# Performance work log

Measured on AMD Instinct MI355X. Metric: run time of the kernel, lower is better.

Reference implementation:

```python
import jax, jax.numpy as jnp
import numpy as np

N_NODES = 50000
N_EDGES = 500000
ATOM_DIM = 128
BOND_DIM = 64
EMB = 128
N_GRAPHS = 256
NUM_LAYER = 2


def _kaiming_uniform(key, fan_out, fan_in):
    # kaiming_uniform_ with nonlinearity='relu': bound = sqrt(6 / fan_in) * sqrt(2)/1 adjustments
    gain = np.sqrt(2.0)
    bound = gain * np.sqrt(3.0 / fan_in)
    return jax.random.uniform(key, (fan_out, fan_in), jnp.float32, -bound, bound)


def setup_inputs() -> dict:
    key = jax.random.key(0)
    ks = jax.random.split(key, 12)
    x = jax.random.normal(ks[0], (N_NODES, ATOM_DIM), jnp.float32)
    edge_attr = jax.random.normal(ks[1], (N_EDGES, BOND_DIM), jnp.float32)
    edge_index = jax.random.randint(ks[2], (2, N_EDGES), 0, N_NODES, jnp.int64)
    batch = jnp.sort(jax.random.randint(ks[3], (N_NODES,), 0, N_GRAPHS, jnp.int64))
    Wa = _kaiming_uniform(ks[4], EMB, ATOM_DIM)
    ba = jnp.zeros((EMB,), jnp.float32)
    Wb = _kaiming_uniform(ks[5], EMB, BOND_DIM)
    bb = jnp.zeros((EMB,), jnp.float32)
    W1 = _kaiming_uniform(ks[6], EMB, EMB)
    b1 = jnp.zeros((EMB,), jnp.float32)
    W2 = _kaiming_uniform(ks[7], EMB // 2, EMB)
    b2 = jnp.zeros((EMB // 2,), jnp.float32)
    W3 = _kaiming_uniform(ks[8], 1, EMB // 2)
    return {"x": x, "edge_attr": edge_attr, "edge_index": edge_index, "batch": batch,
            "Wa": Wa, "ba": ba, "Wb": Wb, "bb": bb,
            "W1": W1, "b1": b1, "W2": W2, "b2": b2, "W3": W3}


def reference(x, edge_attr, edge_index, batch, Wa, ba, Wb, bb, W1, b1, W2, b2, W3):
    src, dst = edge_index[0], edge_index[1]
    # Step 1: embeddings
    node_emb = x @ Wa.T + ba          # [N, EMB]
    edge_emb = edge_attr @ Wb.T + bb  # [E, EMB]
    # Step 2: message passing layers: gather, multiply with edge_emb, scatter-add, residual
    for _ in range(NUM_LAYER):
        msg = node_emb[src] * edge_emb                           # [E, EMB]
        agg = jax.ops.segment_sum(msg, dst, num_segments=N_NODES)  # [N, EMB]
        node_emb = node_emb + agg
    # Step 3: energy MLP (ReLU first, per nn.Sequential)
    h = jax.nn.relu(node_emb)
    h = jax.nn.relu(h @ W1.T + b1)
    h = jax.nn.relu(h @ W2.T + b2)
    node_energy = h @ W3.T            # [N, 1], no bias
    # Step 4: global add pool over graphs
    dg = jax.ops.segment_sum(node_energy, batch, num_segments=N_GRAPHS)  # [G, 1]
    return dg
```

## Files before the change

kernel.cpp:

```cpp
#include <hip/hip_runtime.h>
#include <cstdio>
#include <cstdint>

#define N_NODES 50000
#define N_EDGES 500000
#define EMB 128
#define BOND 64
#define NGRAPH 256
#define NB_SCAN ((N_NODES + 255) / 256)
#define NSTRIP (N_NODES / 16)
#define ESTRIP (N_EDGES / 16)
#define NCHUNK (N_EDGES * BOND / 8)

typedef short bf16x8 __attribute__((ext_vector_type(8)));
typedef unsigned short u16x8 __attribute__((ext_vector_type(8)));
typedef float f32x4  __attribute__((ext_vector_type(4)));

__device__ __forceinline__ unsigned short f2bf(float v){
  unsigned u = __float_as_uint(v);
  unsigned r = (u + 0x7fffu + ((u >> 16) & 1u)) >> 16;
  return (unsigned short)r;
}
__device__ __forceinline__ float bf2f(unsigned short u){
  return __uint_as_float(((unsigned)u) << 16);
}
__device__ __forceinline__ unsigned short brelu(unsigned short u){
  return (u & 0x8000u) ? (unsigned short)0 : u;
}


__global__ void prep_w(const float* __restrict__ Wa, const float* __restrict__ W1,
                       const float* __restrict__ W2, const float* __restrict__ Wb,
                       unsigned short* __restrict__ wabf, unsigned short* __restrict__ w1bf,
                       unsigned short* __restrict__ w2bf, unsigned short* __restrict__ wbbf)
{
  int i = blockIdx.x * 256 + threadIdx.x;
  if (i < 40960){
    int i2 = i & 16383;
    int j = i2 & 7, lb = (i2 >> 3) & 63, kc = (i2 >> 9) & 3, tn = i2 >> 11;
    int lm = lb & 15, q = lb >> 4;
    int row = tn * 16 + lm, col = kc * 32 + q * 8 + j;
    if (i < 16384){
      wabf[i] = f2bf(Wa[row * EMB + col]);
    } else if (i < 32768){
      int pcol = j * 16 + kc * 4 + q;
      w1bf[i2] = f2bf(W1[row * EMB + pcol]);
    } else {
      w2bf[i2] = f2bf(W2[row * EMB + col]);
    }
  } else if (i < 49152){
    int i2 = i - 40960;
    int j = i2 & 7, l = (i2 >> 3) & 63, kc = (i2 >> 9) & 1, tn = i2 >> 10;
    int lm = l & 15, q = l >> 4;
    wbbf[i2] = f2bf(Wb[(tn * 16 + lm) * BOND + kc * 32 + q * 8 + j]);
  }
}

__global__ __launch_bounds__(256) void node_gemm_mfma(const float* __restrict__ x,
    const unsigned short* __restrict__ wabf, const float* __restrict__ ba,
    unsigned short* __restrict__ out)
{
  const int t = threadIdx.x;
  const int wv = t >> 6, l = t & 63;
  const int lm = l & 15, q = l >> 4;
  union U8 { bf16x8 v; unsigned short s[8]; };
  const int strip = blockIdx.x * 4 + wv;
  if (strip >= NSTRIP) return;
  const long n0 = (long)strip * 16;

  bf16x8 a[4];
  #pragma unroll
  for (int kc = 0; kc < 4; kc++){
    const float* ap = x + (n0 + lm) * (long)EMB + kc * 32 + q * 8;
    float4 x0 = *(const float4*)ap;
    float4 x1 = *(const float4*)(ap + 4);
    U8 u;
    u.s[0] = f2bf(x0.x); u.s[1] = f2bf(x0.y); u.s[2] = f2bf(x0.z); u.s[3] = f2bf(x0.w);
    u.s[4] = f2bf(x1.x); u.s[5] = f2bf(x1.y); u.s[6] = f2bf(x1.z); u.s[7] = f2bf(x1.w);
    a[kc] = u.v;
  }
  float biasv[8];
  #pragma unroll
  for (int tn = 0; tn < 8; tn++) biasv[tn] = ba[tn * 16 + lm];

  f32x4 acc[8];
  #pragma unroll
  for (int tn = 0; tn < 8; tn++) acc[tn] = (f32x4){0.f, 0.f, 0.f, 0.f};
  #pragma unroll
  for (int kc = 0; kc < 4; kc++){
    #pragma unroll
    for (int tn = 0; tn < 8; tn++){
      bf16x8 bf = *(const bf16x8*)(wabf + (size_t)((tn * 4 + kc) * 64 + l) * 8);
      acc[tn] = __builtin_amdgcn_mfma_f32_16x16x32_bf16(a[kc], bf, acc[tn], 0, 0, 0);
    }
  }
  #pragma unroll
  for (int i = 0; i < 4; i++){
    U8 o;
    #pragma unroll
    for (int tn = 0; tn < 8; tn++) o.s[tn] = f2bf(acc[tn][i] + biasv[tn]);
    *(bf16x8*)(out + (n0 + q * 4 + i) * (long)EMB + lm * 8) = o.v;
  }
}

__global__ __launch_bounds__(256) void edge_gemm_mfma(
    const unsigned short* __restrict__ attr_bf, const unsigned short* __restrict__ wbbf,
    const float* __restrict__ bb, const int2* __restrict__ cse,
    unsigned short* __restrict__ eemb)
{
  const int t = threadIdx.x;
  const int l = t & 63;
  const int lm = l & 15, q = l >> 4;
  union U8 { bf16x8 v; unsigned short s[8]; };

  bf16x8 bfrag[8][2];
  float bias[8];
  #pragma unroll
  for (int tn = 0; tn < 8; tn++){
    bias[tn] = bb[tn * 16 + lm];
    #pragma unroll
    for (int kc = 0; kc < 2; kc++)
      bfrag[tn][kc] = *(const bf16x8*)(wbbf + (size_t)((tn * 2 + kc) * 64 + l) * 8);
  }

  const long wid = (long)blockIdx.x * 4 + (t >> 6);
  const long stride = (long)gridDim.x * 4 * 16;
  for (long p0 = wid * 16; p0 < N_EDGES; p0 += stride){
    long eid = (long)cse[p0 + lm].y;
    bf16x8 af0 = *(const bf16x8*)(attr_bf + eid * BOND + q * 8);
    bf16x8 af1 = *(const bf16x8*)(attr_bf + eid * BOND + 32 + q * 8);
    f32x4 acc[8];
    #pragma unroll
    for (int tn = 0; tn < 8; tn++) acc[tn] = (f32x4){0.f, 0.f, 0.f, 0.f};
    #pragma unroll
    for (int tn = 0; tn < 8; tn++){
      acc[tn] = __builtin_amdgcn_mfma_f32_16x16x32_bf16(af0, bfrag[tn][0], acc[tn], 0, 0, 0);
      acc[tn] = __builtin_amdgcn_mfma_f32_16x16x32_bf16(af1, bfrag[tn][1], acc[tn], 0, 0, 0);
    }
    #pragma unroll
    for (int i = 0; i < 4; i++){
      U8 o;
      #pragma unroll
      for (int tn = 0; tn < 8; tn++) o.s[tn] = f2bf(acc[tn][i] + bias[tn]);
      *(bf16x8*)(eemb + (p0 + q * 4 + i) * (long)EMB + lm * 8) = o.v;
    }
  }
}


__global__ __launch_bounds__(256) void count_deg_conv(const int* __restrict__ ei,
    int* __restrict__ deg, const float* __restrict__ attr,
    unsigned short* __restrict__ attr_bf)
{
  int id = blockIdx.x * 256 + threadIdx.x;
  if (id < N_EDGES) atomicAdd(&deg[ei[N_EDGES + id]], 1);
  const float* s = attr + (size_t)id * 8;
  float4 a0 = *(const float4*)s;
  float4 a1 = *(const float4*)(s + 4);
  u16x8 o;
  o[0] = f2bf(a0.x); o[1] = f2bf(a0.y); o[2] = f2bf(a0.z); o[3] = f2bf(a0.w);
  o[4] = f2bf(a1.x); o[5] = f2bf(a1.y); o[6] = f2bf(a1.z); o[7] = f2bf(a1.w);
  *(u16x8*)(attr_bf + (size_t)id * 8) = o;
}

__global__ __launch_bounds__(256) void scan_s1(const int* __restrict__ deg,
                                               int* __restrict__ blocksum)
{
  int i = blockIdx.x * 256 + threadIdx.x;
  int lane = threadIdx.x & 63, w = threadIdx.x >> 6;
  int v = (i < N_NODES) ? deg[i] : 0;
  #pragma unroll
  for (int o = 32; o > 0; o >>= 1) v += __shfl_down(v, o, 64);
  __shared__ int ws4[4];
  if (lane == 0) ws4[w] = v;
  __syncthreads();
  if (threadIdx.x == 0) blocksum[blockIdx.x] = ws4[0] + ws4[1] + ws4[2] + ws4[3];
}

__global__ __launch_bounds__(256) void scan_s2(const int* __restrict__ blocksum,
                                               int* __restrict__ blockoff,
                                               int* __restrict__ off)
{
  int t = threadIdx.x;
  int lane = t & 63, w = t >> 6;
  int v = (t < NB_SCAN) ? blocksum[t] : 0;
  int x = v;
  #pragma unroll
  for (int d = 1; d < 64; d <<= 1){
    int y = __shfl_up(x, d, 64);
    if (lane >= d) x += y;
  }
  __shared__ int wsum[4];
  if (lane == 63) wsum[w] = x;
  __syncthreads();
  int wo = 0;
  for (int j = 0; j < w; j++) wo += wsum[j];
  if (t < NB_SCAN) blockoff[t] = wo + x - v;
  if (t == 0) off[N_NODES] = wsum[0] + wsum[1] + wsum[2] + wsum[3];
}

__global__ __launch_bounds__(256) void scan_s3(const int* __restrict__ deg,
    const int* __restrict__ blockoff, int* __restrict__ off, int* __restrict__ fill)
{
  int i = blockIdx.x * 256 + threadIdx.x;
  int lane = threadIdx.x & 63, w = threadIdx.x >> 6;
  int v = (i < N_NODES) ? deg[i] : 0;
  int x = v;
  #pragma unroll
  for (int d = 1; d < 64; d <<= 1){
    int y = __shfl_up(x, d, 64);
    if (lane >= d) x += y;
  }
  __shared__ int wsum[4];
  if (lane == 63) wsum[w] = x;
  __syncthreads();
  int wo = 0;
  for (int j = 0; j < w; j++) wo += wsum[j];
  if (i < N_NODES){
    int excl = blockoff[blockIdx.x] + wo + x - v;
    off[i] = excl;
    fill[i] = excl;
  }
}

__global__ __launch_bounds__(256) void scatter_edges(const int* __restrict__ ei,
    int* __restrict__ fill, int2* __restrict__ cse)
{
  int e = blockIdx.x * 256 + threadIdx.x;
  if (e < N_EDGES){
    int dst = ei[N_EDGES + e];
    int p = atomicAdd(&fill[dst], 1);
    cse[p] = make_int2(ei[e], e);
  }
}

__global__ __launch_bounds__(256) void agg_kernel(const unsigned short* __restrict__ node_old,
    const unsigned short* __restrict__ eemb, const int* __restrict__ off,
    const int2* __restrict__ cse, unsigned short* __restrict__ node_new)
{
  int n = blockIdx.x * 8 + (threadIdx.x >> 5);
  if (n >= N_NODES) return;
  int c0 = (threadIdx.x & 31) * 4;
  int s = off[n], e = off[n + 1];
  ushort4 r = *(const ushort4*)(node_old + (long)n * EMB + c0);
  float4 accA = make_float4(bf2f(r.x), bf2f(r.y), bf2f(r.z), bf2f(r.w));
  float4 accB = make_float4(0.f, 0.f, 0.f, 0.f);
  int i = s;

#define AGG_BLOCK(CNT)                                                        \
  {                                                                           \
    int idx[CNT];                                                             \
    _Pragma("unroll")                                                         \
    for (int j = 0; j < CNT; j++) idx[j] = cse[i + j].x;                      \
    ushort4 a[CNT], eb[CNT];                                                  \
    _Pragma("unroll")                                                         \
    for (int j = 0; j < CNT; j++){                                            \
      a[j]  = *(const ushort4*)(node_old + (long)idx[j] * EMB + c0);          \
      eb[j] = *(const ushort4*)(eemb + (long)(i + j) * EMB + c0);             \
    }                                                                         \
    _Pragma("unroll")                                                         \
    for (int j = 0; j < CNT; j++){                                            \
      float4& acc = (j & 1) ? accB : accA;                                    \
      acc.x = fmaf(bf2f(a[j].x), bf2f(eb[j].x), acc.x);                       \
      acc.y = fmaf(bf2f(a[j].y), bf2f(eb[j].y), acc.y);                       \
      acc.z = fmaf(bf2f(a[j].z), bf2f(eb[j].z), acc.z);                       \
      acc.w = fmaf(bf2f(a[j].w), bf2f(eb[j].w), acc.w);                       \
    }                                                                         \
    i += CNT;                                                                 \
  }

  for (; i + 8 <= e; ) AGG_BLOCK(8)
  if (i + 4 <= e) AGG_BLOCK(4)
  if (i + 2 <= e) AGG_BLOCK(2)
  if (i < e) AGG_BLOCK(1)
#undef AGG_BLOCK

  ushort4 o;
  o.x = f2bf(accA.x + accB.x);
  o.y = f2bf(accA.y + accB.y);
  o.z = f2bf(accA.z + accB.z);
  o.w = f2bf(accA.w + accB.w);
  *(ushort4*)(node_new + (long)n * EMB + c0) = o;
}

__global__ __launch_bounds__(256) void mlp_mfma_pool(const unsigned short* __restrict__ ne,
    const unsigned short* __restrict__ w1bf, const unsigned short* __restrict__ w2bf,
    const float* __restrict__ b1, const float* __restrict__ b2,
    const float* __restrict__ W3, const int* __restrict__ batch,
    float* __restrict__ dg)
{
  __shared__ float h1s[4][16 * 132];
  __shared__ float pool[NGRAPH];
  const int t = threadIdx.x;
  const int wv = t >> 6, l = t & 63;
  const int lm = l & 15, q = l >> 4;
  union U8 { bf16x8 v; unsigned short s[8]; };

  for (int i = t; i < NGRAPH; i += 256) pool[i] = 0.f;
  __syncthreads();

  const int strip = blockIdx.x * 4 + wv;
  if (strip < NSTRIP){
    const long n0 = (long)strip * 16;

    float b1v[8], b2v[4], w3v[4];
    #pragma unroll
    for (int tn = 0; tn < 8; tn++) b1v[tn] = b1[tn * 16 + lm];
    #pragma unroll
    for (int tc = 0; tc < 4; tc++){ b2v[tc] = b2[tc * 16 + lm]; w3v[tc] = W3[tc * 16 + lm]; }

    bf16x8 a1[4];
    #pragma unroll
    for (int kc = 0; kc < 4; kc++){
      const unsigned short* ap = ne + (n0 + lm) * (long)EMB + kc * 32 + q * 8;
      ushort4 v0 = *(const ushort4*)ap;
      ushort4 v1 = *(const ushort4*)(ap + 4);
      U8 u;
      u.s[0] = brelu(v0.x); u.s[1] = brelu(v0.y); u.s[2] = brelu(v0.z); u.s[3] = brelu(v0.w);
      u.s[4] = brelu(v1.x); u.s[5] = brelu(v1.y); u.s[6] = brelu(v1.z); u.s[7] = brelu(v1.w);
      a1[kc] = u.v;
    }

    f32x4 acc1[8];
    #pragma unroll
    for (int tn = 0; tn < 8; tn++) acc1[tn] = (f32x4){b1v[tn], b1v[tn], b1v[tn], b1v[tn]};
    #pragma unroll
    for (int kc = 0; kc < 4; kc++){
      #pragma unroll
      for (int tn = 0; tn < 8; tn++){
        bf16x8 bf = *(const bf16x8*)(w1bf + (size_t)((tn * 4 + kc) * 64 + l) * 8);
        acc1[tn] = __builtin_amdgcn_mfma_f32_16x16x32_bf16(a1[kc], bf, acc1[tn], 0, 0, 0);
      }
    }

    float* h1 = h1s[wv];
    #pragma unroll
    for (int tn = 0; tn < 8; tn++)
      #pragma unroll
      for (int i = 0; i < 4; i++)
        h1[(q * 4 + i) * 132 + tn * 16 + lm] = fmaxf(acc1[tn][i], 0.f);
    bf16x8 a2[4];
    #pragma unroll
    for (int kc = 0; kc < 4; kc++){
      const float* hp = h1 + lm * 132 + kc * 32 + q * 8;
      float4 x0 = *(const float4*)hp;
      float4 x1 = *(const float4*)(hp + 4);
      U8 u;
      u.s[0] = f2bf(x0.x); u.s[1] = f2bf(x0.y); u.s[2] = f2bf(x0.z); u.s[3] = f2bf(x0.w);
      u.s[4] = f2bf(x1.x); u.s[5] = f2bf(x1.y); u.s[6] = f2bf(x1.z); u.s[7] = f2bf(x1.w);
      a2[kc] = u.v;
    }

    f32x4 acc2[4];
    #pragma unroll
    for (int tc = 0; tc < 4; tc++) acc2[tc] = (f32x4){b2v[tc], b2v[tc], b2v[tc], b2v[tc]};
    #pragma unroll
    for (int kc = 0; kc < 4; kc++){
      #pragma unroll
      for (int tc = 0; tc < 4; tc++){
        bf16x8 bf = *(const bf16x8*)(w2bf + (size_t)((tc * 4 + kc) * 64 + l) * 8);
        acc2[tc] = __builtin_amdgcn_mfma_f32_16x16x32_bf16(a2[kc], bf, acc2[tc], 0, 0, 0);
      }
    }

    float e4[4];
    #pragma unroll
    for (int i = 0; i < 4; i++){
      float s = 0.f;
      #pragma unroll
      for (int tc = 0; tc < 4; tc++) s = fmaf(fmaxf(acc2[tc][i], 0.f), w3v[tc], s);
      e4[i] = s;
    }
    #pragma unroll
    for (int m = 1; m < 16; m <<= 1)
      #pragma unroll
      for (int i = 0; i < 4; i++) e4[i] += __shfl_xor(e4[i], m, 64);
    if (lm == 0){
      #pragma unroll
      for (int i = 0; i < 4; i++){
        int node = (int)n0 + q * 4 + i;
        atomicAdd(&pool[batch[node]], e4[i]);
      }
    }
  }
  __syncthreads();
  for (int i = t; i < NGRAPH; i += 256){
    float v = pool[i];
    if (v != 0.f) atomicAdd(&dg[i], v);
  }
}

extern "C" void kernel_launch(void* const* d_in, const int* in_sizes, int n_in,
                              void* d_out, int out_size, void* d_ws, size_t ws_size,
                              hipStream_t stream)
{
  const float* x         = (const float*)d_in[0];
  const float* edge_attr = (const float*)d_in[1];
  const int*   ei        = (const int*)d_in[2];
  const int*   batch     = (const int*)d_in[3];
  const float* Wa = (const float*)d_in[4];
  const float* ba = (const float*)d_in[5];
  const float* Wb = (const float*)d_in[6];
  const float* bb = (const float*)d_in[7];
  const float* W1 = (const float*)d_in[8];
  const float* b1 = (const float*)d_in[9];
  const float* W2 = (const float*)d_in[10];
  const float* b2 = (const float*)d_in[11];
  const float* W3 = (const float*)d_in[12];

  char* ws = (char*)d_ws;
  size_t p = 0;
  auto alloc = [&](size_t bytes) -> char* {
    char* q = ws + p;
    p += (bytes + 255) & ~(size_t)255;
    return q;
  };
  unsigned short* bufA = (unsigned short*)alloc((size_t)N_NODES * EMB * 2);
  unsigned short* bufB = (unsigned short*)alloc((size_t)N_NODES * EMB * 2);
  unsigned short* eemb = (unsigned short*)alloc((size_t)N_EDGES * EMB * 2);
  unsigned short* attr_bf = (unsigned short*)alloc((size_t)N_EDGES * BOND * 2);
  unsigned short* wabf = (unsigned short*)alloc(16384 * sizeof(short));
  unsigned short* w1bf = (unsigned short*)alloc(16384 * sizeof(short));
  unsigned short* w2bf = (unsigned short*)alloc(8192 * sizeof(short));
  unsigned short* wbbf = (unsigned short*)alloc(8192 * sizeof(short));
  int* deg  = (int*)alloc(N_NODES * sizeof(int));
  int* off  = (int*)alloc((N_NODES + 1) * sizeof(int));
  int* fill = (int*)alloc(N_NODES * sizeof(int));
  int* blocksum = (int*)alloc(NB_SCAN * sizeof(int));
  int* blockoff = (int*)alloc(NB_SCAN * sizeof(int));
  int2* cse = (int2*)alloc((size_t)N_EDGES * sizeof(int2));
  if (p > ws_size){
    fprintf(stderr, "kernel_launch: ws too small (%zu < %zu)\n", ws_size, p);
    return;
  }

  hipMemsetAsync(deg, 0, N_NODES * sizeof(int), stream);
  count_deg_conv<<<NCHUNK / 256, 256, 0, stream>>>(ei, deg, edge_attr, attr_bf);
  scan_s1<<<NB_SCAN, 256, 0, stream>>>(deg, blocksum);
  scan_s2<<<1, 256, 0, stream>>>(blocksum, blockoff, off);
  scan_s3<<<NB_SCAN, 256, 0, stream>>>(deg, blockoff, off, fill);
  scatter_edges<<<(N_EDGES + 255) / 256, 256, 0, stream>>>(ei, fill, cse);

  prep_w<<<192, 256, 0, stream>>>(Wa, W1, W2, Wb, wabf, w1bf, w2bf, wbbf);
  node_gemm_mfma<<<(NSTRIP + 3) / 4, 256, 0, stream>>>(x, wabf, ba, bufA);
  edge_gemm_mfma<<<2048, 256, 0, stream>>>(attr_bf, wbbf, bb, cse, eemb);

  agg_kernel<<<(N_NODES + 7) / 8, 256, 0, stream>>>(bufA, eemb, off, cse, bufB);
  agg_kernel<<<(N_NODES + 7) / 8, 256, 0, stream>>>(bufB, eemb, off, cse, bufA);

  hipMemsetAsync(d_out, 0, NGRAPH * sizeof(float), stream);
  mlp_mfma_pool<<<(NSTRIP + 3) / 4, 256, 0, stream>>>(bufA, w1bf, w2bf, b1, b2, W3, batch, (float*)d_out);
}
```

Before: 426.9 us.

## Fuse edge embedding GEMM into per-node aggregation, recomputing edge embeddings per layer

Removes the separate edge GEMM kernel and the materialized bf16 edge-embedding buffer (E x 128). Each message-passing layer now computes edge embeddings on the fly with MFMA from the 64-wide bf16 attributes for each 16-edge chunk of a node's incoming edges, multiplies by gathered source node rows, and reduces across lanes. This avoids writing and twice reading a large edge buffer, at the cost of recomputing the edge GEMM in both layers and running one wave per node, which wastes MFMA lanes on low-degree nodes.

```diff
diff --git a/kernel.cpp b/kernel.cpp
--- a/kernel.cpp
+++ b/kernel.cpp
@@ -9,7 +9,6 @@
 #define NGRAPH 256
 #define NB_SCAN ((N_NODES + 255) / 256)
 #define NSTRIP (N_NODES / 16)
-#define ESTRIP (N_EDGES / 16)
 #define NCHUNK (N_EDGES * BOND / 8)
 
 typedef short bf16x8 __attribute__((ext_vector_type(8)));
@@ -103,50 +102,6 @@
   }
 }
 
-__global__ __launch_bounds__(256) void edge_gemm_mfma(
-    const unsigned short* __restrict__ attr_bf, const unsigned short* __restrict__ wbbf,
-    const float* __restrict__ bb, const int2* __restrict__ cse,
-    unsigned short* __restrict__ eemb)
-{
-  const int t = threadIdx.x;
-  const int l = t & 63;
-  const int lm = l & 15, q = l >> 4;
-  union U8 { bf16x8 v; unsigned short s[8]; };
-
-  bf16x8 bfrag[8][2];
-  float bias[8];
-  #pragma unroll
-  for (int tn = 0; tn < 8; tn++){
-    bias[tn] = bb[tn * 16 + lm];
-    #pragma unroll
-    for (int kc = 0; kc < 2; kc++)
-      bfrag[tn][kc] = *(const bf16x8*)(wbbf + (size_t)((tn * 2 + kc) * 64 + l) * 8);
-  }
-
-  const long wid = (long)blockIdx.x * 4 + (t >> 6);
-  const long stride = (long)gridDim.x * 4 * 16;
-  for (long p0 = wid * 16; p0 < N_EDGES; p0 += stride){
-    long eid = (long)cse[p0 + lm].y;
-    bf16x8 af0 = *(const bf16x8*)(attr_bf + eid * BOND + q * 8);
-    bf16x8 af1 = *(const bf16x8*)(attr_bf + eid * BOND + 32 + q * 8);
-    f32x4 acc[8];
-    #pragma unroll
-    for (int tn = 0; tn < 8; tn++) acc[tn] = (f32x4){0.f, 0.f, 0.f, 0.f};
-    #pragma unroll
-    for (int tn = 0; tn < 8; tn++){
-      acc[tn] = __builtin_amdgcn_mfma_f32_16x16x32_bf16(af0, bfrag[tn][0], acc[tn], 0, 0, 0);
-      acc[tn] = __builtin_amdgcn_mfma_f32_16x16x32_bf16(af1, bfrag[tn][1], acc[tn], 0, 0, 0);
-    }
-    #pragma unroll
-    for (int i = 0; i < 4; i++){
-      U8 o;
-      #pragma unroll
-      for (int tn = 0; tn < 8; tn++) o.s[tn] = f2bf(acc[tn][i] + bias[tn]);
-      *(bf16x8*)(eemb + (p0 + q * 4 + i) * (long)EMB + lm * 8) = o.v;
-    }
-  }
-}
-
 
 __global__ __launch_bounds__(256) void count_deg_conv(const int* __restrict__ ei,
     int* __restrict__ deg, const float* __restrict__ attr,
@@ -234,53 +189,82 @@
   }
 }
 
-__global__ __launch_bounds__(256) void agg_kernel(const unsigned short* __restrict__ node_old,
-    const unsigned short* __restrict__ eemb, const int* __restrict__ off,
+__global__ __launch_bounds__(256) void fused_mp(const unsigned short* __restrict__ node_old,
+    const unsigned short* __restrict__ attr_bf, const unsigned short* __restrict__ wbbf,
+    const float* __restrict__ bb, const int* __restrict__ off,
     const int2* __restrict__ cse, unsigned short* __restrict__ node_new)
 {
-  int n = blockIdx.x * 8 + (threadIdx.x >> 5);
+  const int t = threadIdx.x;
+  const int wv = t >> 6, l = t & 63;
+  const int lm = l & 15, q = l >> 4;
+  union U8 { bf16x8 v; unsigned short s[8]; };
+
+  const int n = blockIdx.x * 4 + wv;
   if (n >= N_NODES) return;
-  int c0 = (threadIdx.x & 31) * 4;
-  int s = off[n], e = off[n + 1];
-  ushort4 r = *(const ushort4*)(node_old + (long)n * EMB + c0);
-  float4 accA = make_float4(bf2f(r.x), bf2f(r.y), bf2f(r.z), bf2f(r.w));
-  float4 accB = make_float4(0.f, 0.f, 0.f, 0.f);
-  int i = s;
-
-#define AGG_BLOCK(CNT)                                                        \
-  {                                                                           \
-    int idx[CNT];                                                             \
-    _Pragma("unroll")                                                         \
-    for (int j = 0; j < CNT; j++) idx[j] = cse[i + j].x;                      \
-    ushort4 a[CNT], eb[CNT];                                                  \
-    _Pragma("unroll")                                                         \
-    for (int j = 0; j < CNT; j++){                                            \
-      a[j]  = *(const ushort4*)(node_old + (long)idx[j] * EMB + c0);          \
-      eb[j] = *(const ushort4*)(eemb + (long)(i + j) * EMB + c0);             \
-    }                                                                         \
-    _Pragma("unroll")                                                         \
-    for (int j = 0; j < CNT; j++){                                            \
-      float4& acc = (j & 1) ? accB : accA;                                    \
-      acc.x = fmaf(bf2f(a[j].x), bf2f(eb[j].x), acc.x);                       \
-      acc.y = fmaf(bf2f(a[j].y), bf2f(eb[j].y), acc.y);                       \
-      acc.z = fmaf(bf2f(a[j].z), bf2f(eb[j].z), acc.z);                       \
-      acc.w = fmaf(bf2f(a[j].w), bf2f(eb[j].w), acc.w);                       \
-    }                                                                         \
-    i += CNT;                                                                 \
-  }
-
-  for (; i + 8 <= e; ) AGG_BLOCK(8)
-  if (i + 4 <= e) AGG_BLOCK(4)
-  if (i + 2 <= e) AGG_BLOCK(2)
-  if (i < e) AGG_BLOCK(1)
-#undef AGG_BLOCK
-
-  ushort4 o;
-  o.x = f2bf(accA.x + accB.x);
-  o.y = f2bf(accA.y + accB.y);
-  o.z = f2bf(accA.z + accB.z);
-  o.w = f2bf(accA.w + accB.w);
-  *(ushort4*)(node_new + (long)n * EMB + c0) = o;
+
+  bf16x8 bfrag[8][2];
+  float bias[8];
+  #pragma unroll
+  for (int tn = 0; tn < 8; tn++){
+    bias[tn] = bb[tn * 16 + lm];
+    bfrag[tn][0] = *(const bf16x8*)(wbbf + (size_t)((tn * 2 + 0) * 64 + l) * 8);
+    bfrag[tn][1] = *(const bf16x8*)(wbbf + (size_t)((tn * 2 + 1) * 64 + l) * 8);
+  }
+
+  const int s = off[n], e = off[n + 1];
+  float lacc[8];
+  #pragma unroll
+  for (int tn = 0; tn < 8; tn++) lacc[tn] = 0.f;
+
+  for (int sb = s; sb < e; sb += 16){
+    int aslot = sb + lm; if (aslot > e - 1) aslot = e - 1;
+    long eid = (long)cse[aslot].y;
+    bf16x8 af0 = *(const bf16x8*)(attr_bf + eid * BOND + q * 8);
+    bf16x8 af1 = *(const bf16x8*)(attr_bf + eid * BOND + 32 + q * 8);
+
+    int srcs[4];
+    #pragma unroll
+    for (int i = 0; i < 4; i++){
+      int slot = sb + q * 4 + i; if (slot > e - 1) slot = e - 1;
+      srcs[i] = cse[slot].x;
+    }
+    U8 ns[4];
+    #pragma unroll
+    for (int i = 0; i < 4; i++)
+      ns[i].v = *(const bf16x8*)(node_old + (long)srcs[i] * EMB + lm * 8);
+
+    f32x4 acc[8];
+    #pragma unroll
+    for (int tn = 0; tn < 8; tn++) acc[tn] = (f32x4){0.f, 0.f, 0.f, 0.f};
+    #pragma unroll
+    for (int tn = 0; tn < 8; tn++){
+      acc[tn] = __builtin_amdgcn_mfma_f32_16x16x32_bf16(af0, bfrag[tn][0], acc[tn], 0, 0, 0);
+      acc[tn] = __builtin_amdgcn_mfma_f32_16x16x32_bf16(af1, bfrag[tn][1], acc[tn], 0, 0, 0);
+    }
+
+    #pragma unroll
+    for (int i = 0; i < 4; i++){
+      if (sb + q * 4 + i < e){
+        #pragma unroll
+        for (int tn = 0; tn < 8; tn++)
+          lacc[tn] = fmaf(acc[tn][i] + bias[tn], bf2f(ns[i].s[tn]), lacc[tn]);
+      }
+    }
+  }
+
+  #pragma unroll
+  for (int tn = 0; tn < 8; tn++){
+    lacc[tn] += __shfl_xor(lacc[tn], 16, 64);
+    lacc[tn] += __shfl_xor(lacc[tn], 32, 64);
+  }
+
+  if (q == 0){
+    U8 r; r.v = *(const bf16x8*)(node_old + (long)n * EMB + lm * 8);
+    U8 o;
+    #pragma unroll
+    for (int tn = 0; tn < 8; tn++) o.s[tn] = f2bf(bf2f(r.s[tn]) + lacc[tn]);
+    *(bf16x8*)(node_new + (long)n * EMB + lm * 8) = o.v;
+  }
 }
 
 __global__ __launch_bounds__(256) void mlp_mfma_pool(const unsigned short* __restrict__ ne,
@@ -417,7 +401,6 @@
   };
   unsigned short* bufA = (unsigned short*)alloc((size_t)N_NODES * EMB * 2);
   unsigned short* bufB = (unsigned short*)alloc((size_t)N_NODES * EMB * 2);
-  unsigned short* eemb = (unsigned short*)alloc((size_t)N_EDGES * EMB * 2);
   unsigned short* attr_bf = (unsigned short*)alloc((size_t)N_EDGES * BOND * 2);
   unsigned short* wabf = (unsigned short*)alloc(16384 * sizeof(short));
   unsigned short* w1bf = (unsigned short*)alloc(16384 * sizeof(short));
@@ -428,7 +411,7 @@
   int* fill = (int*)alloc(N_NODES * sizeof(int));
   int* blocksum = (int*)alloc(NB_SCAN * sizeof(int));
   int* blockoff = (int*)alloc(NB_SCAN * sizeof(int));
-  int2* cse = (int2*)alloc((size_t)N_EDGES * sizeof(int2));
+  int2* cse = (int2*)alloc((size_t)N_EDGES * sizeof(int2) + 256);
   if (p > ws_size){
     fprintf(stderr, "kernel_launch: ws too small (%zu < %zu)\n", ws_size, p);
     return;
@@ -443,10 +426,9 @@
 
   prep_w<<<192, 256, 0, stream>>>(Wa, W1, W2, Wb, wabf, w1bf, w2bf, wbbf);
   node_gemm_mfma<<<(NSTRIP + 3) / 4, 256, 0, stream>>>(x, wabf, ba, bufA);
-  edge_gemm_mfma<<<2048, 256, 0, stream>>>(attr_bf, wbbf, bb, cse, eemb);
-
-  agg_kernel<<<(N_NODES + 7) / 8, 256, 0, stream>>>(bufA, eemb, off, cse, bufB);
-  agg_kernel<<<(N_NODES + 7) / 8, 256, 0, stream>>>(bufB, eemb, off, cse, bufA);
+
+  fused_mp<<<(N_NODES + 3) / 4, 256, 0, stream>>>(bufA, attr_bf, wbbf, bb, off, cse, bufB);
+  fused_mp<<<(N_NODES + 3) / 4, 256, 0, stream>>>(bufB, attr_bf, wbbf, bb, off, cse, bufA);
 
   hipMemsetAsync(d_out, 0, NGRAPH * sizeof(float), stream);
   mlp_mfma_pool<<<(NSTRIP + 3) / 4, 256, 0, stream>>>(bufA, w1bf, w2bf, b1, b2, W3, batch, (float*)d_out);
```

New measurement: 465.2 us. 9.0% more time.
